# Kernel tuning notes

Hardware: AMD Instinct MI355X
Metric: run time of the kernel (lower is better)

## Reference

```python
import jax, jax.numpy as jnp
import numpy as np

D_MODEL = 256
N_LAYERS = 4
D_STATE = 16
EXPAND = 2
D_CONV = 4
D_INNER = EXPAND * D_MODEL
DT_RANK = (D_MODEL + 15) // 16  # ceil(d_model/16) = 16
BATCH = 8
SEQ = 2048
EPS = 1e-5


def setup_inputs() -> dict:
    key = jax.random.key(0)
    ks = jax.random.split(key, 12)
    rn = lambda k, s, sc=0.02: jax.random.normal(k, s, dtype=jnp.float32) * sc
    A_log = jnp.log(jnp.broadcast_to(jnp.arange(1, D_STATE + 1, dtype=jnp.float32),
                                     (N_LAYERS, D_INNER, D_STATE)))
    return {
        "x": jax.random.normal(ks[0], (BATCH, SEQ, 2), dtype=jnp.float32),
        "w_in": rn(ks[1], (D_MODEL, 2), 0.5),
        "b_in": jnp.zeros((D_MODEL,), jnp.float32),
        "norm_w": jnp.ones((N_LAYERS, D_MODEL), jnp.float32),
        "in_proj_w": rn(ks[2], (N_LAYERS, 2 * D_INNER, D_MODEL)),
        "conv_w": rn(ks[3], (N_LAYERS, D_INNER, 1, D_CONV), 0.1),
        "conv_b": jnp.zeros((N_LAYERS, D_INNER), jnp.float32),
        "x_proj_w": rn(ks[4], (N_LAYERS, DT_RANK + 2 * D_STATE, D_INNER)),
        "dt_proj_w": rn(ks[5], (N_LAYERS, D_INNER, DT_RANK), 0.1),
        "dt_proj_b": rn(ks[6], (N_LAYERS, D_INNER), 0.1),
        "A_log": A_log,
        "D_skip": jnp.ones((N_LAYERS, D_INNER), jnp.float32),
        "out_proj_w": rn(ks[7], (N_LAYERS, D_MODEL, D_INNER)),
        "w_head": rn(ks[8], (1, D_MODEL), 0.1),
        "b_head": jnp.zeros((1,), jnp.float32),
    }


def _rmsnorm(x, w):
    return x * jax.lax.rsqrt(jnp.mean(x * x, axis=-1, keepdims=True) + EPS) * w


def _causal_dw_conv(x, w, b):
    # x: (B, L, C); w: (C, 1, K) depthwise; causal left-pad K-1
    xt = jnp.swapaxes(x, 1, 2)  # (B, C, L)
    y = jax.lax.conv_general_dilated(xt, w, (1,), [(D_CONV - 1, 0)],
                                     dimension_numbers=("NCH", "OIH", "NCH"),
                                     feature_group_count=D_INNER)
    return jnp.swapaxes(y + b[None, :, None], 1, 2)


def _selective_scan(u, delta, A, Bm, Cm, Dp):
    # u, delta: (B, L, E); A: (E, N); Bm, Cm: (B, L, N); Dp: (E,)
    dA = jnp.exp(delta[..., None] * A)                 # (B, L, E, N)
    dBu = (delta * u)[..., None] * Bm[:, :, None, :]   # (B, L, E, N)

    def step(h, t):
        dA_t, dBu_t = t
        h = dA_t * h + dBu_t
        return h, h

    h0 = jnp.zeros((u.shape[0], A.shape[0], A.shape[1]), u.dtype)
    _, hs = jax.lax.scan(step, h0, (jnp.swapaxes(dA, 0, 1), jnp.swapaxes(dBu, 0, 1)))
    y = jnp.einsum("lben,bln->ble", hs, Cm)            # (B, L, E)
    return y + u * Dp


def _mamba_block(x, in_w, cw, cb, xp_w, dtw, dtb, A_log, Dp, out_w):
    xz = x @ in_w.T                                    # (B, L, 2E)
    u, z = jnp.split(xz, 2, axis=-1)
    u = jax.nn.silu(_causal_dw_conv(u, cw, cb))
    dbc = u @ xp_w.T                                   # (B, L, dt_rank + 2N)
    delta = jax.nn.softplus(dbc[..., :DT_RANK] @ dtw.T + dtb)
    Bm = dbc[..., DT_RANK:DT_RANK + D_STATE]
    Cm = dbc[..., DT_RANK + D_STATE:]
    y = _selective_scan(u, delta, -jnp.exp(A_log), Bm, Cm, Dp)
    return (y * jax.nn.silu(z)) @ out_w.T


def reference(x, w_in, b_in, norm_w, in_proj_w, conv_w, conv_b, x_proj_w,
              dt_proj_w, dt_proj_b, A_log, D_skip, out_proj_w, w_head, b_head):
    h = x @ w_in.T + b_in                              # (B, L, d_model)
    for i in range(N_LAYERS):
        h = h + _mamba_block(_rmsnorm(h, norm_w[i]), in_proj_w[i], conv_w[i],
                             conv_b[i], x_proj_w[i], dt_proj_w[i], dt_proj_b[i],
                             A_log[i], D_skip[i], out_proj_w[i])
    return (h @ w_head.T + b_head)[..., 0]             # (B, L)
```

## Files before the change

kernel.cpp:

```cpp
#include <hip/hip_runtime.h>
#include <hip/hip_bf16.h>

#define BATCH 8
#define SEQ   2048
#define DM    256
#define DI    512
#define DS    16
#define DTR   16
#define NL    4
#define ROWS  (BATCH*SEQ)
#define NCH   32
#define CHL   64
#define NF    576

typedef __attribute__((ext_vector_type(8))) __bf16 bh8;
typedef __attribute__((ext_vector_type(4))) float f4;

#if __has_builtin(__builtin_amdgcn_exp2f)
#define EXP2(x) __builtin_amdgcn_exp2f(x)
#else
#define EXP2(x) exp2f(x)
#endif
#define LOG2E 1.4426950408889634f

__device__ __forceinline__ float bf2f(unsigned short u) {
    union { unsigned int i; float f; } v; v.i = ((unsigned int)u) << 16; return v.f;
}
__device__ __forceinline__ float4 us4f(ushort4 q) {
    return make_float4(bf2f(q.x), bf2f(q.y), bf2f(q.z), bf2f(q.w));
}
__device__ __forceinline__ float ldg1(const void* p, int i, int bf) {
    if (bf) return bf2f(((const unsigned short*)p)[i]);
    return ((const float*)p)[i];
}
__device__ __forceinline__ float4 ldg4(const void* p, int i, int bf) {
    if (bf) return us4f(*(const ushort4*)(((const unsigned short*)p) + i));
    return *(const float4*)(((const float*)p) + i);
}
__device__ __forceinline__ unsigned short f2bs(float f) {
    union { float f; unsigned u; } x; x.f = f;
    unsigned r = (x.u + 0x7fffu + ((x.u >> 16) & 1u)) >> 16;
    return (unsigned short)r;
}
__device__ __forceinline__ float fsilu(float x) {
    return x * __builtin_amdgcn_rcpf(1.0f + __expf(-x));
}
__device__ __forceinline__ float fsoftplus(float x) {
    return (x > 15.0f) ? x : __logf(1.0f + __expf(x));
}
__device__ __forceinline__ void pow16(float e1, float* pw) {
    float p2 = e1 * e1, p3 = p2 * e1, p4 = p2 * p2;
    float p5 = p4 * e1, p6 = p4 * p2, p7 = p4 * p3, p8 = p4 * p4;
    pw[0] = e1; pw[1] = p2; pw[2] = p3; pw[3] = p4;
    pw[4] = p5; pw[5] = p6; pw[6] = p7; pw[7] = p8;
    pw[8]  = p8 * e1; pw[9]  = p8 * p2; pw[10] = p8 * p3; pw[11] = p8 * p4;
    pw[12] = p8 * p5; pw[13] = p8 * p6; pw[14] = p8 * p7; pw[15] = p8 * p8;
}

__global__ void k_probe(const void* x, const void* A_log, int* flag) {
    int t = threadIdx.x;
    float v = bf2f(((const unsigned short*)x)[2 * t]);
    int bad = (fabsf(v) < 32.0f) ? 0 : 1;
    for (int o = 1; o < 64; o <<= 1) bad += __shfl_xor(bad, o);
    int bf = (bad > 8) ? 0 : 1;
    int nb = 0;
    for (int j = 0; j < 64; j++) {
        int e = ((j * 64 + t) * 17) & 32767;
        int n = e & 15;
        float a = ldg1(A_log, e, bf);
        float ea = __expf(a);
        if (fabsf(ea - (float)(n + 1)) > 0.02f * (float)(n + 1)) nb = 1;
    }
    for (int o = 1; o < 64; o <<= 1) nb += __shfl_xor(nb, o);
    if (t == 0) { flag[0] = bf; flag[1] = (nb == 0) ? 1 : 0; }
}

__global__ __launch_bounds__(256) void k_prep(const void* dtw, const void* xpw,
                                              unsigned short* Wc, const int* flag) {
    int bf = *flag;
    int blk = blockIdx.x;
    int l = blk / NF, r = blk % NF;
    int t = threadIdx.x;
    unsigned short* out = Wc + ((size_t)l * NF + r) * DI;
#pragma unroll
    for (int p = 0; p < 2; p++) {
        int k = t + p * 256;
        float v = 0.0f;
        if (r < 512) {
            const int db = l * DI * DTR + r * DTR;
            const int xb = l * 48 * DI;
#pragma unroll
            for (int j = 0; j < 16; j++)
                v = fmaf(ldg1(dtw, db + j, bf), ldg1(xpw, xb + j * DI + k, bf), v);
        } else if (r < 544) {
            v = ldg1(xpw, l * 48 * DI + (16 + r - 512) * DI + k, bf);
        }
        out[k] = f2bs(v);
    }
}

__global__ __launch_bounds__(256) void k_inproj(const void* x, const void* w_in,
                                                const void* b_in, unsigned short* h, const int* flag) {
    int bf = *flag;
    int row = blockIdx.x, e = threadIdx.x;
    float x0 = ldg1(x, row * 2 + 0, bf), x1 = ldg1(x, row * 2 + 1, bf);
    float w0 = ldg1(w_in, e * 2 + 0, bf), w1 = ldg1(w_in, e * 2 + 1, bf);
    float bb = ldg1(b_in, e, bf);
    h[(size_t)row * DM + e] = f2bs(fmaf(x0, w0, fmaf(x1, w1, bb)));
}

__global__ __launch_bounds__(256) void k_rmsnorm(const unsigned short* h, const void* norm_w,
                                                 int w_off, unsigned short* xn, const int* flag) {
    int bf = *flag;
    int wv = threadIdx.x >> 6, ln = threadIdx.x & 63;
    int row = blockIdx.x * 4 + wv;
    float4 v = us4f(*(const ushort4*)(h + (size_t)row * DM + ln * 4));
    float ss = v.x * v.x + v.y * v.y + v.z * v.z + v.w * v.w;
    for (int o = 1; o < 64; o <<= 1) ss += __shfl_xor(ss, o);
    float sc = rsqrtf(ss / DM + 1e-5f);
    float4 w = ldg4(norm_w, w_off + ln * 4, bf);
    ushort4 o4 = { f2bs(v.x * sc * w.x), f2bs(v.y * sc * w.y),
                   f2bs(v.z * sc * w.z), f2bs(v.w * sc * w.w) };
    *(ushort4*)(xn + (size_t)row * DM + ln * 4) = o4;
}

#define ASTR 72

template <int BN, bool ADD>
__global__ __launch_bounds__(256, 4) void k_mfma(const unsigned short* A, const void* W, int w_off,
                                                 unsigned short* Cp, int N, int K, const int* flag) {
    int bf = *flag;
    __shared__ unsigned short SMEM[(128 + BN) * ASTR];
    unsigned short* As = SMEM;
    unsigned short* Ws = SMEM + 128 * ASTR;
    constexpr int NT = BN / 32;
    constexpr int WCH = BN * 8 / 256;
    constexpr int TSTR = BN + 8;

    int bm = blockIdx.x, bn = blockIdx.y;
    int t = threadIdx.x;
    int w = t >> 6, lane = t & 63;
    int wm = w >> 1, wn = w & 1;
    int lr = lane & 15, quad = lane >> 4;

    f4 acc[4][NT];
#pragma unroll
    for (int i = 0; i < 4; i++)
#pragma unroll
        for (int j = 0; j < NT; j++) acc[i][j] = f4{0.f, 0.f, 0.f, 0.f};

    for (int k0 = 0; k0 < K; k0 += 64) {
        __syncthreads();
#pragma unroll
        for (int i = 0; i < 4; i++) {
            int ch = t + i * 256;
            int r = ch >> 3, kc = (ch & 7) * 8;
            *(uint4*)&As[r * ASTR + kc] =
                *(const uint4*)(A + (size_t)(bm * 128 + r) * K + k0 + kc);
        }
#pragma unroll
        for (int i = 0; i < WCH; i++) {
            int ch = t + i * 256;
            int r = ch >> 3, kc = (ch & 7) * 8;
            size_t off = (size_t)w_off + (size_t)(bn * BN + r) * K + k0 + kc;
            if (bf) {
                *(uint4*)&Ws[r * ASTR + kc] = *(const uint4*)((const unsigned short*)W + off);
            } else {
                const float* src = (const float*)W + off;
                float4 a0 = *(const float4*)src;
                float4 a1 = *(const float4*)(src + 4);
                ushort4 v0 = { f2bs(a0.x), f2bs(a0.y), f2bs(a0.z), f2bs(a0.w) };
                ushort4 v1 = { f2bs(a1.x), f2bs(a1.y), f2bs(a1.z), f2bs(a1.w) };
                *(ushort4*)&Ws[r * ASTR + kc] = v0;
                *(ushort4*)&Ws[r * ASTR + kc + 4] = v1;
            }
        }
        __syncthreads();
#pragma unroll
        for (int ks = 0; ks < 64; ks += 32) {
            bh8 af[4];
#pragma unroll
            for (int i = 0; i < 4; i++)
                af[i] = *(const bh8*)&As[(wm * 64 + i * 16 + lr) * ASTR + ks + quad * 8];
            bh8 wf[NT];
#pragma unroll
            for (int j = 0; j < NT; j++)
                wf[j] = *(const bh8*)&Ws[(wn * (BN / 2) + j * 16 + lr) * ASTR + ks + quad * 8];
#pragma unroll
            for (int i = 0; i < 4; i++)
#pragma unroll
                for (int j = 0; j < NT; j++)
                    acc[i][j] = __builtin_amdgcn_mfma_f32_16x16x32_bf16(af[i], wf[j], acc[i][j], 0, 0, 0);
        }
    }
    __syncthreads();
    unsigned short* Tile = SMEM;
#pragma unroll
    for (int i = 0; i < 4; i++) {
        int rl = wm * 64 + i * 16 + quad * 4;
#pragma unroll
        for (int j = 0; j < NT; j++) {
            int cl = wn * (BN / 2) + j * 16 + lr;
#pragma unroll
            for (int r = 0; r < 4; r++)
                Tile[(rl + r) * TSTR + cl] = f2bs(acc[i][j][r]);
        }
    }
    __syncthreads();
    constexpr int CPT = 128 * BN / 8 / 256;
#pragma unroll
    for (int i = 0; i < CPT; i++) {
        int ch = t + i * 256;
        int r = ch / (BN / 8), qc = (ch % (BN / 8)) * 8;
        uint4 v = *(uint4*)&Tile[r * TSTR + qc];
        size_t gidx = (size_t)(bm * 128 + r) * N + bn * BN + qc;
        if (ADD) {
            uint4 c = *(uint4*)&Cp[gidx];
            unsigned short* vp = (unsigned short*)&v;
            unsigned short* cp2 = (unsigned short*)&c;
            uint4 o;
            unsigned short* op = (unsigned short*)&o;
#pragma unroll
            for (int e = 0; e < 8; e++) op[e] = f2bs(bf2f(vp[e]) + bf2f(cp2[e]));
            *(uint4*)&Cp[gidx] = o;
        } else {
            *(uint4*)&Cp[gidx] = v;
        }
    }
}

__global__ __launch_bounds__(256, 4) void k_fused(const unsigned short* A, const unsigned short* Wc,
                                                  int w_off, unsigned short* delta, float* BC,
                                                  const void* dtb, int layer, const int* flag) {
    int bf = *flag;
    __shared__ unsigned short SMEM[(128 + 64) * ASTR];
    unsigned short* As = SMEM;
    unsigned short* Ws = SMEM + 128 * ASTR;
    constexpr int TSTR = 72;

    int bm = blockIdx.x, bn = blockIdx.y;
    int t = threadIdx.x;
    int w = t >> 6, lane = t & 63;
    int wm = w >> 1, wn = w & 1;
    int lr = lane & 15, quad = lane >> 4;

    f4 acc[4][2];
#pragma unroll
    for (int i = 0; i < 4; i++)
#pragma unroll
        for (int j = 0; j < 2; j++) acc[i][j] = f4{0.f, 0.f, 0.f, 0.f};

    for (int k0 = 0; k0 < DI; k0 += 64) {
        __syncthreads();
#pragma unroll
        for (int i = 0; i < 4; i++) {
            int ch = t + i * 256;
            int r = ch >> 3, kc = (ch & 7) * 8;
            *(uint4*)&As[r * ASTR + kc] =
                *(const uint4*)(A + (size_t)(bm * 128 + r) * DI + k0 + kc);
        }
#pragma unroll
        for (int i = 0; i < 2; i++) {
            int ch = t + i * 256;
            int r = ch >> 3, kc = (ch & 7) * 8;
            *(uint4*)&Ws[r * ASTR + kc] =
                *(const uint4*)(Wc + (size_t)w_off + (size_t)(bn * 64 + r) * DI + k0 + kc);
        }
        __syncthreads();
#pragma unroll
        for (int ks = 0; ks < 64; ks += 32) {
            bh8 af[4];
#pragma unroll
            for (int i = 0; i < 4; i++)
                af[i] = *(const bh8*)&As[(wm * 64 + i * 16 + lr) * ASTR + ks + quad * 8];
            bh8 wf[2];
#pragma unroll
            for (int j = 0; j < 2; j++)
                wf[j] = *(const bh8*)&Ws[(wn * 32 + j * 16 + lr) * ASTR + ks + quad * 8];
#pragma unroll
            for (int i = 0; i < 4; i++)
#pragma unroll
                for (int j = 0; j < 2; j++)
                    acc[i][j] = __builtin_amdgcn_mfma_f32_16x16x32_bf16(af[i], wf[j], acc[i][j], 0, 0, 0);
        }
    }
    if (bn < 8) {
        __syncthreads();
        unsigned short* Tile = SMEM;
#pragma unroll
        for (int i = 0; i < 4; i++) {
            int rl = wm * 64 + i * 16 + quad * 4;
#pragma unroll
            for (int j = 0; j < 2; j++) {
                int cl = wn * 32 + j * 16 + lr;
                float bb = ldg1(dtb, layer * DI + bn * 64 + cl, bf);
#pragma unroll
                for (int r = 0; r < 4; r++)
                    Tile[(rl + r) * TSTR + cl] = f2bs(fsoftplus(acc[i][j][r] + bb));
            }
        }
        __syncthreads();
#pragma unroll
        for (int i = 0; i < 4; i++) {
            int ch = t + i * 256;
            int r = ch >> 3, qc = (ch & 7) * 8;
            uint4 v = *(uint4*)&Tile[r * TSTR + qc];
            *(uint4*)&delta[(size_t)(bm * 128 + r) * DI + bn * 64 + qc] = v;
        }
    } else {
#pragma unroll
        for (int i = 0; i < 4; i++) {
            int row0 = bm * 128 + wm * 64 + i * 16 + quad * 4;
#pragma unroll
            for (int j = 0; j < 2; j++) {
                int col = bn * 64 + wn * 32 + j * 16 + lr;
                if (col < 544) {
#pragma unroll
                    for (int r = 0; r < 4; r++)
                        BC[(size_t)(row0 + r) * 32 + (col - 512)] = acc[i][j][r];
                }
            }
        }
    }
}

__global__ __launch_bounds__(256) void k_conv(const unsigned short* xz, const void* cw, const void* cb,
                                              int layer, unsigned short* u, const int* flag) {
    int bf = *flag;
    int idx = blockIdx.x * 256 + threadIdx.x;
    int dq = idx & 127;
    int row = idx >> 7;
    int l = row & (SEQ - 1);
    int d = dq * 4;
    float4 w0 = ldg4(cw, (layer * DI + d + 0) * 4, bf);
    float4 w1 = ldg4(cw, (layer * DI + d + 1) * 4, bf);
    float4 w2 = ldg4(cw, (layer * DI + d + 2) * 4, bf);
    float4 w3 = ldg4(cw, (layer * DI + d + 3) * 4, bf);
    float4 bb = ldg4(cb, layer * DI + d, bf);
    const unsigned short* base = xz + (size_t)row * (2 * DI) + d;
    float4 t0 = make_float4(0, 0, 0, 0), t1 = t0, t2 = t0;
    if (l >= 3) t0 = us4f(*(const ushort4*)(base - 3 * 2 * DI));
    if (l >= 2) t1 = us4f(*(const ushort4*)(base - 2 * 2 * DI));
    if (l >= 1) t2 = us4f(*(const ushort4*)(base - 1 * 2 * DI));
    float4 t3 = us4f(*(const ushort4*)base);
    float a0 = bb.x; a0 = fmaf(w0.x, t0.x, a0); a0 = fmaf(w0.y, t1.x, a0); a0 = fmaf(w0.z, t2.x, a0); a0 = fmaf(w0.w, t3.x, a0);
    float a1 = bb.y; a1 = fmaf(w1.x, t0.y, a1); a1 = fmaf(w1.y, t1.y, a1); a1 = fmaf(w1.z, t2.y, a1); a1 = fmaf(w1.w, t3.y, a1);
    float a2 = bb.z; a2 = fmaf(w2.x, t0.z, a2); a2 = fmaf(w2.y, t1.z, a2); a2 = fmaf(w2.z, t2.z, a2); a2 = fmaf(w2.w, t3.z, a2);
    float a3 = bb.w; a3 = fmaf(w3.x, t0.w, a3); a3 = fmaf(w3.y, t1.w, a3); a3 = fmaf(w3.z, t2.w, a3); a3 = fmaf(w3.w, t3.w, a3);
    ushort4 o = { f2bs(fsilu(a0)), f2bs(fsilu(a1)), f2bs(fsilu(a2)), f2bs(fsilu(a3)) };
    *(ushort4*)(u + (size_t)row * DI + d) = o;
}

__global__ __launch_bounds__(256) void k_scan1(const unsigned short* delta, const unsigned short* u,
                                               const float* BC, const void* A_log, float* Sb, float* E,
                                               int layer, const int* flag) {
    int bf = flag[0], sA = flag[1];
    int x = blockIdx.x;
    int dg = x & 1, c = (x >> 1) & (NCH - 1), b = x >> 6;
    int tid = threadIdx.x;
    int d = dg * 256 + tid;
    int t0 = c * CHL;

    __shared__ float sB[CHL][16];
    {
        int r = tid >> 2, q = tid & 3;
        *(float4*)&sB[r][q * 4] =
            *(const float4*)(BC + ((size_t)b * SEQ + t0 + r) * 32 + q * 4);
    }

    float A2[16];
#pragma unroll
    for (int n4 = 0; n4 < 4; n4++) {
        float4 a4 = ldg4(A_log, (layer * DI + d) * DS + n4 * 4, bf);
        A2[n4 * 4 + 0] = -__expf(a4.x) * LOG2E;
        A2[n4 * 4 + 1] = -__expf(a4.y) * LOG2E;
        A2[n4 * 4 + 2] = -__expf(a4.z) * LOG2E;
        A2[n4 * 4 + 3] = -__expf(a4.w) * LOG2E;
    }
    float h[16];
#pragma unroll
    for (int n = 0; n < 16; n++) h[n] = 0.0f;
    float S = 0.0f;

    const unsigned short* dp = delta + ((size_t)b * SEQ + t0) * DI + d;
    const unsigned short* up = u + ((size_t)b * SEQ + t0) * DI + d;

    float dl0[4], uu0[4];
#pragma unroll
    for (int j = 0; j < 4; j++) { dl0[j] = bf2f(dp[j * DI]); uu0[j] = bf2f(up[j * DI]); }
    __syncthreads();

    for (int s = 0; s < CHL / 4; s++) {
        int sn = (s + 1 < CHL / 4) ? (s + 1) : s;
        float dl1[4], uu1[4];
#pragma unroll
        for (int j = 0; j < 4; j++) {
            dl1[j] = bf2f(dp[(sn * 4 + j) * DI]);
            uu1[j] = bf2f(up[(sn * 4 + j) * DI]);
        }
#pragma unroll
        for (int j = 0; j < 4; j++) {
            int t = s * 4 + j;
            float dlt = dl0[j], uu = uu0[j];
            float du = dlt * uu;
            S += dlt;
            if (sA) {
                float pw[16];
                pow16(EXP2(-dlt * LOG2E), pw);
#pragma unroll
                for (int n4 = 0; n4 < 4; n4++) {
                    float4 Bv = *(const float4*)&sB[t][n4 * 4];
                    int n = n4 * 4;
                    h[n + 0] = fmaf(pw[n + 0], h[n + 0], du * Bv.x);
                    h[n + 1] = fmaf(pw[n + 1], h[n + 1], du * Bv.y);
                    h[n + 2] = fmaf(pw[n + 2], h[n + 2], du * Bv.z);
                    h[n + 3] = fmaf(pw[n + 3], h[n + 3], du * Bv.w);
                }
            } else {
#pragma unroll
                for (int n4 = 0; n4 < 4; n4++) {
                    float4 Bv = *(const float4*)&sB[t][n4 * 4];
                    int n = n4 * 4;
                    float a0 = EXP2(dlt * A2[n + 0]); h[n + 0] = fmaf(a0, h[n + 0], du * Bv.x);
                    float a1 = EXP2(dlt * A2[n + 1]); h[n + 1] = fmaf(a1, h[n + 1], du * Bv.y);
                    float a2 = EXP2(dlt * A2[n + 2]); h[n + 2] = fmaf(a2, h[n + 2], du * Bv.z);
                    float a3 = EXP2(dlt * A2[n + 3]); h[n + 3] = fmaf(a3, h[n + 3], du * Bv.w);
                }
            }
        }
#pragma unroll
        for (int j = 0; j < 4; j++) { dl0[j] = dl1[j]; uu0[j] = uu1[j]; }
    }
    Sb[((size_t)b * NCH + c) * DI + d] = S;
    float* Ed = E + (((size_t)b * NCH + c) * DI + d) * DS;
#pragma unroll
    for (int n4 = 0; n4 < 4; n4++)
        *(float4*)(Ed + n4 * 4) = make_float4(h[n4 * 4], h[n4 * 4 + 1], h[n4 * 4 + 2], h[n4 * 4 + 3]);
}

__global__ __launch_bounds__(256) void k_stitch(const float* Sb, const void* A_log, float* E,
                                                int layer, const int* flag) {
    int bf = flag[0];
    int g = blockIdx.x * 256 + threadIdx.x;
    int b = g >> 13, r = g & 8191;
    int d = r >> 4;
    float A2a = -__expf(ldg1(A_log, (layer * DI + d) * DS + (r & 15), bf)) * LOG2E;
    size_t ebase = (size_t)b * NCH * (DI * DS) + r;
    float H = 0.0f;
    for (int c = 0; c < NCH; c++) {
        float p = EXP2(A2a * Sb[((size_t)b * NCH + c) * DI + d]);
        size_t idx = ebase + (size_t)c * (DI * DS);
        float e = E[idx];
        E[idx] = H;
        H = fmaf(p, H, e);
    }
}

__global__ __launch_bounds__(256) void k_scan2(const unsigned short* delta, const unsigned short* u,
                                               const float* BC, const void* A_log, const void* D_skip,
                                               const unsigned short* xz, const float* E,
                                               unsigned short* g, int layer, const int* flag) {
    int bf = flag[0], sA = flag[1];
    int x = blockIdx.x;
    int dg = x & 1, c = (x >> 1) & (NCH - 1), b = x >> 6;
    int tid = threadIdx.x;
    int d = dg * 256 + tid;
    int t0 = c * CHL;

    __shared__ float sBC[CHL][32];
#pragma unroll
    for (int k2 = 0; k2 < 2; k2++) {
        int fi = k2 * 256 + tid;
        int r = fi >> 3, q = fi & 7;
        *(float4*)&sBC[r][q * 4] =
            *(const float4*)(BC + ((size_t)b * SEQ + t0 + r) * 32 + q * 4);
    }

    float A2[16];
#pragma unroll
    for (int n4 = 0; n4 < 4; n4++) {
        float4 a4 = ldg4(A_log, (layer * DI + d) * DS + n4 * 4, bf);
        A2[n4 * 4 + 0] = -__expf(a4.x) * LOG2E;
        A2[n4 * 4 + 1] = -__expf(a4.y) * LOG2E;
        A2[n4 * 4 + 2] = -__expf(a4.z) * LOG2E;
        A2[n4 * 4 + 3] = -__expf(a4.w) * LOG2E;
    }
    float Dp = ldg1(D_skip, layer * DI + d, bf);

    float h[16];
    const float* E0 = E + (((size_t)b * NCH + c) * DI + d) * DS;
#pragma unroll
    for (int n4 = 0; n4 < 4; n4++) {
        float4 h4 = *(const float4*)(E0 + n4 * 4);
        h[n4 * 4 + 0] = h4.x; h[n4 * 4 + 1] = h4.y; h[n4 * 4 + 2] = h4.z; h[n4 * 4 + 3] = h4.w;
    }

    const unsigned short* dp = delta + ((size_t)b * SEQ + t0) * DI + d;
    const unsigned short* up = u + ((size_t)b * SEQ + t0) * DI + d;
    const unsigned short* zp = xz + ((size_t)b * SEQ + t0) * (2 * DI) + DI + d;
    unsigned short* gp = g + ((size_t)b * SEQ + t0) * DI + d;

    float dl0[4], uu0[4], zz0[4];
#pragma unroll
    for (int j = 0; j < 4; j++) {
        dl0[j] = bf2f(dp[j * DI]); uu0[j] = bf2f(up[j * DI]); zz0[j] = bf2f(zp[j * (2 * DI)]);
    }
    __syncthreads();

    for (int s = 0; s < CHL / 4; s++) {
        int sn = (s + 1 < CHL / 4) ? (s + 1) : s;
        float dl1[4], uu1[4], zz1[4];
#pragma unroll
        for (int j = 0; j < 4; j++) {
            dl1[j] = bf2f(dp[(sn * 4 + j) * DI]);
            uu1[j] = bf2f(up[(sn * 4 + j) * DI]);
            zz1[j] = bf2f(zp[(sn * 4 + j) * (2 * DI)]);
        }
#pragma unroll
        for (int j = 0; j < 4; j++) {
            int t = s * 4 + j;
            float dlt = dl0[j], uu = uu0[j], zz = zz0[j];
            float du = dlt * uu;
            float y = 0.0f;
            if (sA) {
                float pw[16];
                pow16(EXP2(-dlt * LOG2E), pw);
#pragma unroll
                for (int n4 = 0; n4 < 4; n4++) {
                    float4 Bv = *(const float4*)&sBC[t][n4 * 4];
                    float4 Cv = *(const float4*)&sBC[t][16 + n4 * 4];
                    int n = n4 * 4;
                    h[n + 0] = fmaf(pw[n + 0], h[n + 0], du * Bv.x); y = fmaf(Cv.x, h[n + 0], y);
                    h[n + 1] = fmaf(pw[n + 1], h[n + 1], du * Bv.y); y = fmaf(Cv.y, h[n + 1], y);
                    h[n + 2] = fmaf(pw[n + 2], h[n + 2], du * Bv.z); y = fmaf(Cv.z, h[n + 2], y);
                    h[n + 3] = fmaf(pw[n + 3], h[n + 3], du * Bv.w); y = fmaf(Cv.w, h[n + 3], y);
                }
            } else {
#pragma unroll
                for (int n4 = 0; n4 < 4; n4++) {
                    float4 Bv = *(const float4*)&sBC[t][n4 * 4];
                    float4 Cv = *(const float4*)&sBC[t][16 + n4 * 4];
                    int n = n4 * 4;
                    float a0 = EXP2(dlt * A2[n + 0]); h[n + 0] = fmaf(a0, h[n + 0], du * Bv.x); y = fmaf(Cv.x, h[n + 0], y);
                    float a1 = EXP2(dlt * A2[n + 1]); h[n + 1] = fmaf(a1, h[n + 1], du * Bv.y); y = fmaf(Cv.y, h[n + 1], y);
                    float a2 = EXP2(dlt * A2[n + 2]); h[n + 2] = fmaf(a2, h[n + 2], du * Bv.z); y = fmaf(Cv.z, h[n + 2], y);
                    float a3 = EXP2(dlt * A2[n + 3]); h[n + 3] = fmaf(a3, h[n + 3], du * Bv.w); y = fmaf(Cv.w, h[n + 3], y);
                }
            }
            float yt = fmaf(uu, Dp, y);
            gp[(size_t)t * DI] = f2bs(yt * fsilu(zz));
        }
#pragma unroll
        for (int j = 0; j < 4; j++) { dl0[j] = dl1[j]; uu0[j] = uu1[j]; zz0[j] = zz1[j]; }
    }
}

__global__ __launch_bounds__(256) void k_head(const unsigned short* h, const void* w_head,
                                              const void* b_head, void* out, const int* flag) {
    int bf = *flag;
    int wv = threadIdx.x >> 6, ln = threadIdx.x & 63;
    int row = blockIdx.x * 4 + wv;
    float4 v = us4f(*(const ushort4*)(h + (size_t)row * DM + ln * 4));
    float4 w = ldg4(w_head, ln * 4, bf);
    float s = v.x * w.x + v.y * w.y + v.z * w.z + v.w * w.w;
    for (int o = 1; o < 64; o <<= 1) s += __shfl_xor(s, o);
    if (ln == 0) {
        s += ldg1(b_head, 0, bf);
        if (bf) ((__hip_bfloat16*)out)[row] = __float2bfloat16(s);
        else    ((float*)out)[row] = s;
    }
}

extern "C" void kernel_launch(void* const* d_in, const int* in_sizes, int n_in,
                              void* d_out, int out_size, void* d_ws, size_t ws_size,
                              hipStream_t stream) {
    (void)in_sizes; (void)n_in; (void)out_size; (void)ws_size;
    const void* x      = d_in[0];
    const void* w_in   = d_in[1];
    const void* b_in   = d_in[2];
    const void* norm_w = d_in[3];
    const void* ipw    = d_in[4];
    const void* cw     = d_in[5];
    const void* cb     = d_in[6];
    const void* xpw    = d_in[7];
    const void* dtw    = d_in[8];
    const void* dtb    = d_in[9];
    const void* A_log  = d_in[10];
    const void* D_skip = d_in[11];
    const void* opw    = d_in[12];
    const void* w_head = d_in[13];
    const void* b_head = d_in[14];

    float* ws    = (float*)d_ws;
    unsigned short* h     = (unsigned short*)ws;
    unsigned short* xn    = (unsigned short*)(ws + 4194304);
    float*          Sb    = ws + 4194304;
    float*          E     = ws + 4718592;
    unsigned short* xz    = (unsigned short*)(ws + 8388608);
    unsigned short* u     = (unsigned short*)(ws + 25165824);
    float*          BC    = ws + 33554432;
    unsigned short* delta = (unsigned short*)(ws + 34340864);
    unsigned short* Wcomb = (unsigned short*)(ws + 38535168);
    int*            flag  = (int*)(ws + 42729472);

    k_probe<<<1, 64, 0, stream>>>(x, A_log, flag);
    k_prep<<<NL * NF, 256, 0, stream>>>(dtw, xpw, Wcomb, flag);
    k_inproj<<<ROWS, 256, 0, stream>>>(x, w_in, b_in, h, flag);

    for (int layer = 0; layer < NL; layer++) {
        k_rmsnorm<<<ROWS / 4, 256, 0, stream>>>(h, norm_w, layer * DM, xn, flag);
        k_mfma<128, false><<<dim3(ROWS / 128, 2 * DI / 128), 256, 0, stream>>>(
            xn, ipw, layer * 2 * DI * DM, xz, 2 * DI, DM, flag);
        k_conv<<<ROWS * DI / 4 / 256, 256, 0, stream>>>(xz, cw, cb, layer, u, flag);
        k_fused<<<dim3(ROWS / 128, NF / 64), 256, 0, stream>>>(
            u, Wcomb, layer * NF * DI, delta, BC, dtb, layer, flag);
        k_scan1<<<BATCH * NCH * 2, 256, 0, stream>>>(delta, u, BC, A_log, Sb, E, layer, flag);
        k_stitch<<<BATCH * DI * DS / 256, 256, 0, stream>>>(Sb, A_log, E, layer, flag);
        k_scan2<<<BATCH * NCH * 2, 256, 0, stream>>>(delta, u, BC, A_log, D_skip, xz, E,
                                                     u , layer, flag);
        k_mfma<64, true><<<dim3(ROWS / 128, DM / 64), 256, 0, stream>>>(
            u, opw, layer * DM * DI, h, DM, DI, flag);
    }

    k_head<<<ROWS / 4, 256, 0, stream>>>(h, w_head, b_head, d_out, flag);
}
```

Baseline: 635.8 us.

## Fuse chunked scan passes into one cooperative kernel with grid syncs

Merges the three scan stages (per-chunk scan, cross-chunk stitch, output scan) into a single cooperative kernel separated by grid-wide syncs. Each block stages its delta and u chunk in shared memory once, so the second pass reuses them instead of reloading from global memory, and two launches per layer are removed. This needs all 512 blocks to be co-resident, which rests on the occupancy hint of two blocks per CU and the roughly 73 KB of shared memory per block. It also adds grid-sync overhead, and the stitch phase runs on only half the blocks while the rest wait.

Result: slower. 1.621 ms (+155.0%).

```diff
diff --git a/kernel.cpp b/kernel.cpp
--- a/kernel.cpp
+++ b/kernel.cpp
@@ -1,5 +1,8 @@
 #include <hip/hip_runtime.h>
 #include <hip/hip_bf16.h>
+#include <hip/hip_cooperative_groups.h>
+
+namespace cg = cooperative_groups;
 
 #define BATCH 8
 #define SEQ   2048
@@ -351,9 +354,13 @@
     *(ushort4*)(u + (size_t)row * DI + d) = o;
 }
 
-__global__ __launch_bounds__(256) void k_scan1(const unsigned short* delta, const unsigned short* u,
-                                               const float* BC, const void* A_log, float* Sb, float* E,
-                                               int layer, const int* flag) {
+__global__ __launch_bounds__(256, 2) void k_scan_fused(
+    const unsigned short* __restrict__ delta, const unsigned short* __restrict__ u,
+    const float* __restrict__ BC, const void* __restrict__ A_log,
+    const void* __restrict__ D_skip, const unsigned short* __restrict__ xz,
+    float* __restrict__ Sb, float* __restrict__ E, unsigned short* __restrict__ g,
+    int layer, const int* __restrict__ flag) {
+    cg::grid_group grid = cg::this_grid();
     int bf = flag[0], sA = flag[1];
     int x = blockIdx.x;
     int dg = x & 1, c = (x >> 1) & (NCH - 1), b = x >> 6;
@@ -361,11 +368,27 @@
     int d = dg * 256 + tid;
     int t0 = c * CHL;
 
-    __shared__ float sB[CHL][16];
+    __shared__ unsigned short sD[CHL][256];
+    __shared__ unsigned short sU[CHL][256];
+    __shared__ float sBC[CHL][32];
+
     {
-        int r = tid >> 2, q = tid & 3;
-        *(float4*)&sB[r][q * 4] =
-            *(const float4*)(BC + ((size_t)b * SEQ + t0 + r) * 32 + q * 4);
+        const unsigned short* dgl = delta + ((size_t)b * SEQ + t0) * DI + dg * 256;
+        const unsigned short* ugl = u + ((size_t)b * SEQ + t0) * DI + dg * 256;
+#pragma unroll
+        for (int i = 0; i < 8; i++) {
+            int ch = i * 256 + tid;
+            int r = ch >> 5, qc = (ch & 31) * 8;
+            *(uint4*)&sD[r][qc] = *(const uint4*)(dgl + (size_t)r * DI + qc);
+            *(uint4*)&sU[r][qc] = *(const uint4*)(ugl + (size_t)r * DI + qc);
+        }
+#pragma unroll
+        for (int i = 0; i < 2; i++) {
+            int fi = i * 256 + tid;
+            int r = fi >> 3, q = fi & 7;
+            *(float4*)&sBC[r][q * 4] =
+                *(const float4*)(BC + ((size_t)b * SEQ + t0 + r) * 32 + q * 4);
+        }
     }
 
     float A2[16];
@@ -377,31 +400,17 @@
         A2[n4 * 4 + 2] = -__expf(a4.z) * LOG2E;
         A2[n4 * 4 + 3] = -__expf(a4.w) * LOG2E;
     }
-    float h[16];
-#pragma unroll
-    for (int n = 0; n < 16; n++) h[n] = 0.0f;
-    float S = 0.0f;
-
-    const unsigned short* dp = delta + ((size_t)b * SEQ + t0) * DI + d;
-    const unsigned short* up = u + ((size_t)b * SEQ + t0) * DI + d;
-
-    float dl0[4], uu0[4];
-#pragma unroll
-    for (int j = 0; j < 4; j++) { dl0[j] = bf2f(dp[j * DI]); uu0[j] = bf2f(up[j * DI]); }
     __syncthreads();
 
-    for (int s = 0; s < CHL / 4; s++) {
-        int sn = (s + 1 < CHL / 4) ? (s + 1) : s;
-        float dl1[4], uu1[4];
-#pragma unroll
-        for (int j = 0; j < 4; j++) {
-            dl1[j] = bf2f(dp[(sn * 4 + j) * DI]);
-            uu1[j] = bf2f(up[(sn * 4 + j) * DI]);
-        }
-#pragma unroll
-        for (int j = 0; j < 4; j++) {
-            int t = s * 4 + j;
-            float dlt = dl0[j], uu = uu0[j];
+    {
+        float h[16];
+#pragma unroll
+        for (int n = 0; n < 16; n++) h[n] = 0.0f;
+        float S = 0.0f;
+#pragma unroll 4
+        for (int t = 0; t < CHL; t++) {
+            float dlt = bf2f(sD[t][tid]);
+            float uu  = bf2f(sU[t][tid]);
             float du = dlt * uu;
             S += dlt;
             if (sA) {
@@ -409,7 +418,7 @@
                 pow16(EXP2(-dlt * LOG2E), pw);
 #pragma unroll
                 for (int n4 = 0; n4 < 4; n4++) {
-                    float4 Bv = *(const float4*)&sB[t][n4 * 4];
+                    float4 Bv = *(const float4*)&sBC[t][n4 * 4];
                     int n = n4 * 4;
                     h[n + 0] = fmaf(pw[n + 0], h[n + 0], du * Bv.x);
                     h[n + 1] = fmaf(pw[n + 1], h[n + 1], du * Bv.y);
@@ -419,7 +428,7 @@
             } else {
 #pragma unroll
                 for (int n4 = 0; n4 < 4; n4++) {
-                    float4 Bv = *(const float4*)&sB[t][n4 * 4];
+                    float4 Bv = *(const float4*)&sBC[t][n4 * 4];
                     int n = n4 * 4;
                     float a0 = EXP2(dlt * A2[n + 0]); h[n + 0] = fmaf(a0, h[n + 0], du * Bv.x);
                     float a1 = EXP2(dlt * A2[n + 1]); h[n + 1] = fmaf(a1, h[n + 1], du * Bv.y);
@@ -428,130 +437,97 @@
                 }
             }
         }
-#pragma unroll
-        for (int j = 0; j < 4; j++) { dl0[j] = dl1[j]; uu0[j] = uu1[j]; }
-    }
-    Sb[((size_t)b * NCH + c) * DI + d] = S;
-    float* Ed = E + (((size_t)b * NCH + c) * DI + d) * DS;
-#pragma unroll
-    for (int n4 = 0; n4 < 4; n4++)
-        *(float4*)(Ed + n4 * 4) = make_float4(h[n4 * 4], h[n4 * 4 + 1], h[n4 * 4 + 2], h[n4 * 4 + 3]);
-}
-
-__global__ __launch_bounds__(256) void k_stitch(const float* Sb, const void* A_log, float* E,
-                                                int layer, const int* flag) {
-    int bf = flag[0];
-    int g = blockIdx.x * 256 + threadIdx.x;
-    int b = g >> 13, r = g & 8191;
-    int d = r >> 4;
-    float A2a = -__expf(ldg1(A_log, (layer * DI + d) * DS + (r & 15), bf)) * LOG2E;
-    size_t ebase = (size_t)b * NCH * (DI * DS) + r;
-    float H = 0.0f;
-    for (int c = 0; c < NCH; c++) {
-        float p = EXP2(A2a * Sb[((size_t)b * NCH + c) * DI + d]);
-        size_t idx = ebase + (size_t)c * (DI * DS);
-        float e = E[idx];
-        E[idx] = H;
-        H = fmaf(p, H, e);
-    }
-}
-
-__global__ __launch_bounds__(256) void k_scan2(const unsigned short* delta, const unsigned short* u,
-                                               const float* BC, const void* A_log, const void* D_skip,
-                                               const unsigned short* xz, const float* E,
-                                               unsigned short* g, int layer, const int* flag) {
-    int bf = flag[0], sA = flag[1];
-    int x = blockIdx.x;
-    int dg = x & 1, c = (x >> 1) & (NCH - 1), b = x >> 6;
-    int tid = threadIdx.x;
-    int d = dg * 256 + tid;
-    int t0 = c * CHL;
-
-    __shared__ float sBC[CHL][32];
-#pragma unroll
-    for (int k2 = 0; k2 < 2; k2++) {
-        int fi = k2 * 256 + tid;
-        int r = fi >> 3, q = fi & 7;
-        *(float4*)&sBC[r][q * 4] =
-            *(const float4*)(BC + ((size_t)b * SEQ + t0 + r) * 32 + q * 4);
-    }
-
-    float A2[16];
-#pragma unroll
-    for (int n4 = 0; n4 < 4; n4++) {
-        float4 a4 = ldg4(A_log, (layer * DI + d) * DS + n4 * 4, bf);
-        A2[n4 * 4 + 0] = -__expf(a4.x) * LOG2E;
-        A2[n4 * 4 + 1] = -__expf(a4.y) * LOG2E;
-        A2[n4 * 4 + 2] = -__expf(a4.z) * LOG2E;
-        A2[n4 * 4 + 3] = -__expf(a4.w) * LOG2E;
-    }
-    float Dp = ldg1(D_skip, layer * DI + d, bf);
-
-    float h[16];
-    const float* E0 = E + (((size_t)b * NCH + c) * DI + d) * DS;
-#pragma unroll
-    for (int n4 = 0; n4 < 4; n4++) {
-        float4 h4 = *(const float4*)(E0 + n4 * 4);
-        h[n4 * 4 + 0] = h4.x; h[n4 * 4 + 1] = h4.y; h[n4 * 4 + 2] = h4.z; h[n4 * 4 + 3] = h4.w;
-    }
-
-    const unsigned short* dp = delta + ((size_t)b * SEQ + t0) * DI + d;
-    const unsigned short* up = u + ((size_t)b * SEQ + t0) * DI + d;
-    const unsigned short* zp = xz + ((size_t)b * SEQ + t0) * (2 * DI) + DI + d;
-    unsigned short* gp = g + ((size_t)b * SEQ + t0) * DI + d;
-
-    float dl0[4], uu0[4], zz0[4];
-#pragma unroll
-    for (int j = 0; j < 4; j++) {
-        dl0[j] = bf2f(dp[j * DI]); uu0[j] = bf2f(up[j * DI]); zz0[j] = bf2f(zp[j * (2 * DI)]);
-    }
-    __syncthreads();
-
-    for (int s = 0; s < CHL / 4; s++) {
-        int sn = (s + 1 < CHL / 4) ? (s + 1) : s;
-        float dl1[4], uu1[4], zz1[4];
-#pragma unroll
-        for (int j = 0; j < 4; j++) {
-            dl1[j] = bf2f(dp[(sn * 4 + j) * DI]);
-            uu1[j] = bf2f(up[(sn * 4 + j) * DI]);
-            zz1[j] = bf2f(zp[(sn * 4 + j) * (2 * DI)]);
-        }
-#pragma unroll
-        for (int j = 0; j < 4; j++) {
-            int t = s * 4 + j;
-            float dlt = dl0[j], uu = uu0[j], zz = zz0[j];
-            float du = dlt * uu;
-            float y = 0.0f;
-            if (sA) {
-                float pw[16];
-                pow16(EXP2(-dlt * LOG2E), pw);
-#pragma unroll
-                for (int n4 = 0; n4 < 4; n4++) {
-                    float4 Bv = *(const float4*)&sBC[t][n4 * 4];
-                    float4 Cv = *(const float4*)&sBC[t][16 + n4 * 4];
-                    int n = n4 * 4;
-                    h[n + 0] = fmaf(pw[n + 0], h[n + 0], du * Bv.x); y = fmaf(Cv.x, h[n + 0], y);
-                    h[n + 1] = fmaf(pw[n + 1], h[n + 1], du * Bv.y); y = fmaf(Cv.y, h[n + 1], y);
-                    h[n + 2] = fmaf(pw[n + 2], h[n + 2], du * Bv.z); y = fmaf(Cv.z, h[n + 2], y);
-                    h[n + 3] = fmaf(pw[n + 3], h[n + 3], du * Bv.w); y = fmaf(Cv.w, h[n + 3], y);
+        Sb[((size_t)b * NCH + c) * DI + d] = S;
+        float* Ed = E + (((size_t)b * NCH + c) * DI + d) * DS;
+#pragma unroll
+        for (int n4 = 0; n4 < 4; n4++)
+            *(float4*)(Ed + n4 * 4) =
+                make_float4(h[n4 * 4], h[n4 * 4 + 1], h[n4 * 4 + 2], h[n4 * 4 + 3]);
+    }
+
+    __threadfence();
+    grid.sync();
+
+    if (x < 256) {
+        int gg = x * 256 + tid;
+        int b2 = gg >> 13, r2 = gg & 8191;
+        int d2 = r2 >> 4;
+        float A2a = -__expf(ldg1(A_log, (layer * DI + d2) * DS + (r2 & 15), bf)) * LOG2E;
+        size_t ebase = (size_t)b2 * NCH * (DI * DS) + r2;
+        float H = 0.0f;
+        for (int cc = 0; cc < NCH; cc++) {
+            float p = EXP2(A2a * Sb[((size_t)b2 * NCH + cc) * DI + d2]);
+            size_t idx = ebase + (size_t)cc * (DI * DS);
+            float e = E[idx];
+            E[idx] = H;
+            H = fmaf(p, H, e);
+        }
+    }
+
+    __threadfence();
+    grid.sync();
+
+    {
+        float Dp = ldg1(D_skip, layer * DI + d, bf);
+        float h[16];
+        const float* E0 = E + (((size_t)b * NCH + c) * DI + d) * DS;
+#pragma unroll
+        for (int n4 = 0; n4 < 4; n4++) {
+            float4 h4 = *(const float4*)(E0 + n4 * 4);
+            h[n4 * 4 + 0] = h4.x; h[n4 * 4 + 1] = h4.y;
+            h[n4 * 4 + 2] = h4.z; h[n4 * 4 + 3] = h4.w;
+        }
+        const unsigned short* zp = xz + ((size_t)b * SEQ + t0) * (2 * DI) + DI + d;
+        unsigned short* gp = g + ((size_t)b * SEQ + t0) * DI + d;
+
+        float zz0[4];
+#pragma unroll
+        for (int j = 0; j < 4; j++) zz0[j] = bf2f(zp[j * (2 * DI)]);
+
+        for (int s = 0; s < CHL / 4; s++) {
+            int sn = (s + 1 < CHL / 4) ? (s + 1) : s;
+            float zz1[4];
+#pragma unroll
+            for (int j = 0; j < 4; j++) zz1[j] = bf2f(zp[(sn * 4 + j) * (2 * DI)]);
+#pragma unroll
+            for (int j = 0; j < 4; j++) {
+                int t = s * 4 + j;
+                float dlt = bf2f(sD[t][tid]);
+                float uu  = bf2f(sU[t][tid]);
+                float zz = zz0[j];
+                float du = dlt * uu;
+                float y = 0.0f;
+                if (sA) {
+                    float pw[16];
+                    pow16(EXP2(-dlt * LOG2E), pw);
+#pragma unroll
+                    for (int n4 = 0; n4 < 4; n4++) {
+                        float4 Bv = *(const float4*)&sBC[t][n4 * 4];
+                        float4 Cv = *(const float4*)&sBC[t][16 + n4 * 4];
+                        int n = n4 * 4;
+                        h[n + 0] = fmaf(pw[n + 0], h[n + 0], du * Bv.x); y = fmaf(Cv.x, h[n + 0], y);
+                        h[n + 1] = fmaf(pw[n + 1], h[n + 1], du * Bv.y); y = fmaf(Cv.y, h[n + 1], y);
+                        h[n + 2] = fmaf(pw[n + 2], h[n + 2], du * Bv.z); y = fmaf(Cv.z, h[n + 2], y);
+                        h[n + 3] = fmaf(pw[n + 3], h[n + 3], du * Bv.w); y = fmaf(Cv.w, h[n + 3], y);
+                    }
+                } else {
+#pragma unroll
+                    for (int n4 = 0; n4 < 4; n4++) {
+                        float4 Bv = *(const float4*)&sBC[t][n4 * 4];
+                        float4 Cv = *(const float4*)&sBC[t][16 + n4 * 4];
+                        int n = n4 * 4;
+                        float a0 = EXP2(dlt * A2[n + 0]); h[n + 0] = fmaf(a0, h[n + 0], du * Bv.x); y = fmaf(Cv.x, h[n + 0], y);
+                        float a1 = EXP2(dlt * A2[n + 1]); h[n + 1] = fmaf(a1, h[n + 1], du * Bv.y); y = fmaf(Cv.y, h[n + 1], y);
+                        float a2 = EXP2(dlt * A2[n + 2]); h[n + 2] = fmaf(a2, h[n + 2], du * Bv.z); y = fmaf(Cv.z, h[n + 2], y);
+                        float a3 = EXP2(dlt * A2[n + 3]); h[n + 3] = fmaf(a3, h[n + 3], du * Bv.w); y = fmaf(Cv.w, h[n + 3], y);
+                    }
                 }
-            } else {
-#pragma unroll
-                for (int n4 = 0; n4 < 4; n4++) {
-                    float4 Bv = *(const float4*)&sBC[t][n4 * 4];
-                    float4 Cv = *(const float4*)&sBC[t][16 + n4 * 4];
-                    int n = n4 * 4;
-                    float a0 = EXP2(dlt * A2[n + 0]); h[n + 0] = fmaf(a0, h[n + 0], du * Bv.x); y = fmaf(Cv.x, h[n + 0], y);
-                    float a1 = EXP2(dlt * A2[n + 1]); h[n + 1] = fmaf(a1, h[n + 1], du * Bv.y); y = fmaf(Cv.y, h[n + 1], y);
-                    float a2 = EXP2(dlt * A2[n + 2]); h[n + 2] = fmaf(a2, h[n + 2], du * Bv.z); y = fmaf(Cv.z, h[n + 2], y);
-                    float a3 = EXP2(dlt * A2[n + 3]); h[n + 3] = fmaf(a3, h[n + 3], du * Bv.w); y = fmaf(Cv.w, h[n + 3], y);
-                }
+                float yt = fmaf(uu, Dp, y);
+                gp[(size_t)t * DI] = f2bs(yt * fsilu(zz));
             }
-            float yt = fmaf(uu, Dp, y);
-            gp[(size_t)t * DI] = f2bs(yt * fsilu(zz));
-        }
-#pragma unroll
-        for (int j = 0; j < 4; j++) { dl0[j] = dl1[j]; uu0[j] = uu1[j]; zz0[j] = zz1[j]; }
+#pragma unroll
+            for (int j = 0; j < 4; j++) zz0[j] = zz1[j];
+        }
     }
 }
 
@@ -614,10 +590,22 @@
         k_conv<<<ROWS * DI / 4 / 256, 256, 0, stream>>>(xz, cw, cb, layer, u, flag);
         k_fused<<<dim3(ROWS / 128, NF / 64), 256, 0, stream>>>(
             u, Wcomb, layer * NF * DI, delta, BC, dtb, layer, flag);
-        k_scan1<<<BATCH * NCH * 2, 256, 0, stream>>>(delta, u, BC, A_log, Sb, E, layer, flag);
-        k_stitch<<<BATCH * DI * DS / 256, 256, 0, stream>>>(Sb, A_log, E, layer, flag);
-        k_scan2<<<BATCH * NCH * 2, 256, 0, stream>>>(delta, u, BC, A_log, D_skip, xz, E,
-                                                     u , layer, flag);
+        {
+            const unsigned short* a0 = delta;
+            const unsigned short* a1 = u;
+            const float*          a2 = BC;
+            const void*           a3 = A_log;
+            const void*           a4 = D_skip;
+            const unsigned short* a5 = xz;
+            float*                a6 = Sb;
+            float*                a7 = E;
+            unsigned short*       a8 = u;
+            int                   a9 = layer;
+            const int*            a10 = flag;
+            void* kargs[] = { &a0, &a1, &a2, &a3, &a4, &a5, &a6, &a7, &a8, &a9, &a10 };
+            hipLaunchCooperativeKernel((void*)k_scan_fused, dim3(BATCH * NCH * 2), dim3(256),
+                                       kargs, 0, stream);
+        }
         k_mfma<64, true><<<dim3(ROWS / 128, DM / 64), 256, 0, stream>>>(
             u, opw, layer * DM * DI, h, DM, DI, flag);
     }
```
